# Optimization experiments

Measured on AMD Instinct MI355X. Metric: run time of the kernel, lower is better.

Reference implementation:

```python
import jax, jax.numpy as jnp
import numpy as np

B, S, D_MODEL = 2, 2048, 1024
HID, D_FF, H, WIN = 256, 512, 4, 9
LN_EPS = 1e-5


def setup_inputs() -> dict:
    key = jax.random.key(0)
    ks = jax.random.split(key, 12)
    w = lambda k, shape: jax.random.normal(k, shape, jnp.float32) * 0.02
    return dict(
        q=jax.random.normal(ks[0], (B, S, D_MODEL), jnp.float32),
        k=jax.random.normal(ks[1], (B, S, D_MODEL), jnp.float32),
        v=jax.random.normal(ks[2], (B, S, D_MODEL), jnp.float32),
        Wq=w(ks[3], (D_MODEL, HID)), bq=jnp.zeros((HID,), jnp.float32),
        Wk=w(ks[4], (D_MODEL, HID)), bk=jnp.zeros((HID,), jnp.float32),
        Wv=w(ks[5], (D_MODEL, HID)), bv=jnp.zeros((HID,), jnp.float32),
        Wo=w(ks[6], (HID, D_MODEL)), bo=jnp.zeros((D_MODEL,), jnp.float32),
        alpha=jnp.zeros((1,), jnp.float32),
        adj_w=jnp.full((1,), 0.6, jnp.float32),
        adj_b=jnp.full((1,), 0.2, jnp.float32),
        W1=w(ks[7], (D_MODEL, D_FF)), b1=jnp.zeros((D_FF,), jnp.float32),
        W2=w(ks[8], (D_FF, D_MODEL)), b2=jnp.zeros((D_MODEL,), jnp.float32),
        g1=jnp.ones((D_MODEL,), jnp.float32), be1=jnp.zeros((D_MODEL,), jnp.float32),
        g2=jnp.ones((D_MODEL,), jnp.float32), be2=jnp.zeros((D_MODEL,), jnp.float32),
    )


def _layernorm(x, g, b):
    mu = jnp.mean(x, axis=-1, keepdims=True)
    var = jnp.mean((x - mu) ** 2, axis=-1, keepdims=True)
    return (x - mu) * jax.lax.rsqrt(var + LN_EPS) * g + b


def _signed_sqrt(x):
    # sqrt(relu(x)) - sqrt(relu(-x)) with torch-style zero grad on masked branch
    p = jnp.where(x > 0, jnp.sqrt(jnp.where(x > 0, x, 1.0)), 0.0)
    n = jnp.where(x < 0, jnp.sqrt(jnp.where(x < 0, -x, 1.0)), 0.0)
    return p - n


def _local_mask(seq_len, win):
    j = jnp.arange(seq_len)[:, None]              # [S,1]
    kk = jnp.arange(win)[None, :]                 # [1,W]
    idx = jnp.clip(j - win // 2 + kk, 0, seq_len - 1)
    m = jnp.zeros((seq_len, seq_len), jnp.float32)
    return m.at[jnp.broadcast_to(j, (seq_len, win)), idx].set(1.0)


def _forward(q, k, v, Wq, bq, Wk, bk, Wv, bv, Wo, bo, alpha, adj_w, adj_b,
             W1, b1, W2, b2, g1, be1, g2, be2):
    bs, seq, _ = q.shape
    dh = HID // H
    scale = 1.0 / np.sqrt(HID)

    Q = (q @ Wq + bq).reshape(bs, seq, H, dh).transpose(0, 2, 1, 3)  # [B,H,S,dh]
    K = (k @ Wk + bk).reshape(bs, seq, H, dh).transpose(0, 2, 1, 3)
    V = (v @ Wv + bv).reshape(bs, seq, H, dh).transpose(0, 2, 1, 3)

    # distance adjacency bias: exp(-|w*d^2 - b|), d = |i-j|
    i = jnp.arange(seq, dtype=jnp.float32)
    dist = jnp.abs(i[:, None] - i[None, :])
    adj = jnp.exp(-jnp.abs(adj_w[0] * dist ** 2 - adj_b[0]))  # [S,S]

    scores = jnp.einsum('bhqd,bhkd->bhqk', Q, K) * scale + adj  # [B,H,S,S]

    mask = _local_mask(seq, WIN)                                 # [S,S]
    l_scores = jnp.where(mask == 0, -1e9, scores)

    g_map = jax.nn.softmax(scores, axis=-1)
    l_map = jax.nn.softmax(l_scores, axis=-1)

    glb = jnp.einsum('bhqk,bhkd->bqhd', g_map, V).reshape(bs, seq, HID)
    lcl = jnp.einsum('bhqk,bhkd->bqhd', l_map, V).reshape(bs, seq, HID)

    a = jax.nn.sigmoid(alpha[0])
    tmp = a * glb + (1.0 - a) * lcl

    # norm_flag: signed sqrt then F.normalize (L2 along dim=1, eps=1e-12)
    tmp = _signed_sqrt(tmp)
    nrm = jnp.maximum(jnp.sqrt(jnp.sum(tmp ** 2, axis=1, keepdims=True)), 1e-12)
    tmp = tmp / nrm

    attn_out = tmp @ Wo + bo

    x = q + attn_out
    x = _layernorm(x, g1, be1)
    # FFN (dropout inactive in eval)
    x = x + (jax.nn.relu(x @ W1 + b1) @ W2 + b2)
    x = _layernorm(x, g2, be2)
    return x


def reference(q, k, v, Wq, bq, Wk, bk, Wv, bv, Wo, bo, alpha, adj_w, adj_b,
              W1, b1, W2, b2, g1, be1, g2, be2):
    return _forward(q, k, v, Wq, bq, Wk, bk, Wv, bv, Wo, bo, alpha, adj_w,
                    adj_b, W1, b1, W2, b2, g1, be1, g2, be2)
```

## Files before the change

### kernel.cpp

```cpp
#include <hip/hip_runtime.h>

#define B_SZ   2
#define S_LEN  2048
#define DMODEL 1024
#define HID    256
#define NH     4
#define DH     64
#define DFF    512
#define LN_EPS 1e-5f
#define ATT_SCALE 0.0625f

typedef __attribute__((ext_vector_type(8))) short bf16x8;
typedef __attribute__((ext_vector_type(4))) float f32x4;

static __device__ __forceinline__ unsigned short f2bf(float x) {
    union { float f; unsigned u; } v; v.f = x;
    unsigned r = v.u + 0x7FFFu + ((v.u >> 16) & 1u);
    return (unsigned short)(r >> 16);
}
static __device__ __forceinline__ unsigned packbf(float a, float b) {
    return (unsigned)f2bf(a) | ((unsigned)f2bf(b) << 16);
}
static __device__ __forceinline__ float bf2f(unsigned short h) {
    union { unsigned u; float f; } v; v.u = ((unsigned)h) << 16; return v.f;
}
static __device__ __forceinline__ int swz(int byte) {
    return byte ^ ((byte >> 3) & 0x70);
}

#if defined(__has_builtin)
#if __has_builtin(__builtin_amdgcn_global_load_lds)
#define HAVE_GLD 1
#endif
#endif

static __device__ __forceinline__ void gld16(const void* g, void* l) {
#ifdef HAVE_GLD
    __builtin_amdgcn_global_load_lds(
        (const __attribute__((address_space(1))) void*)g,
        (__attribute__((address_space(3))) void*)l, 16, 0, 0);
#else
    *(uint4*)((char*)l + (threadIdx.x & 63) * 16) = *(const uint4*)g;
#endif
}

__device__ __forceinline__ void gstage(const unsigned short* __restrict__ G,
                                       int row0, int k0, int K, char* lds, int lane)
{
    #pragma unroll
    for (int j = 0; j < 8; ++j) {
        int o = (j * 64 + lane) * 16;
        int L = o ^ ((o >> 3) & 0x70);
        const char* ga = (const char*)G +
            ((size_t)(row0 + (L >> 7)) * K + k0) * 2 + (L & 127);
        gld16(ga, lds + j * 1024);
    }
}

__device__ __forceinline__ void gcompute(const char* As, const char* Bs,
                                         f32x4 acc[4][4], int lr, int lg)
{
    #pragma unroll
    for (int ks = 0; ks < 2; ++ks) {
        bf16x8 af[4], bfv[4];
        #pragma unroll
        for (int m = 0; m < 4; ++m) {
            int r = m * 16 + lr;
            af[m] = *(const bf16x8*)(As + ((r * 128 + ks * 64 + lg * 16) ^ ((lr & 7) << 4)));
        }
        #pragma unroll
        for (int n = 0; n < 4; ++n) {
            int r = n * 16 + lr;
            bfv[n] = *(const bf16x8*)(Bs + ((r * 128 + ks * 64 + lg * 16) ^ ((lr & 7) << 4)));
        }
        #pragma unroll
        for (int m = 0; m < 4; ++m)
            #pragma unroll
            for (int n = 0; n < 4; ++n)
                acc[m][n] = __builtin_amdgcn_mfma_f32_16x16x32_bf16(
                    af[m], bfv[n], acc[m][n], 0, 0, 0);
    }
}

__device__ __forceinline__ void gemm64_core(
    const unsigned short* __restrict__ A, const unsigned short* __restrict__ W,
    const float* __restrict__ bias, const float* __restrict__ residf,
    const unsigned short* __restrict__ residb,
    float* __restrict__ Cf, unsigned short* __restrict__ Cb,
    int N, int K, int relu, int row0, int col0)
{
    __shared__ char As0[8192], As1[8192], Bs0[8192], Bs1[8192];
    const int lane = threadIdx.x;
    const int lr = lane & 15, lg = lane >> 4;

    f32x4 acc[4][4] = {};

    gstage(A, row0, 0, K, As0, lane);
    gstage(W, col0, 0, K, Bs0, lane);
    const int NK = K >> 6;
    for (int ks = 0; ks + 2 < NK; ks += 2) {
        gstage(A, row0, (ks + 1) * 64, K, As1, lane);
        gstage(W, col0, (ks + 1) * 64, K, Bs1, lane);
        gcompute(As0, Bs0, acc, lr, lg);
        gstage(A, row0, (ks + 2) * 64, K, As0, lane);
        gstage(W, col0, (ks + 2) * 64, K, Bs0, lane);
        gcompute(As1, Bs1, acc, lr, lg);
    }
    gstage(A, row0, (NK - 1) * 64, K, As1, lane);
    gstage(W, col0, (NK - 1) * 64, K, Bs1, lane);
    gcompute(As0, Bs0, acc, lr, lg);
    gcompute(As1, Bs1, acc, lr, lg);

    #pragma unroll
    for (int mf = 0; mf < 4; ++mf) {
        #pragma unroll
        for (int nf = 0; nf < 4; ++nf) {
            #pragma unroll
            for (int r = 0; r < 4; ++r) {
                int row = row0 + mf * 16 + lg * 4 + r;
                int col = col0 + nf * 16 + lr;
                float v2 = acc[mf][nf][r] + bias[col];
                if (residf) v2 += residf[(size_t)row * N + col];
                if (residb) v2 += bf2f(residb[(size_t)row * N + col]);
                if (relu)   v2 = fmaxf(v2, 0.f);
                if (Cb) Cb[(size_t)row * N + col] = f2bf(v2);
                else    Cf[(size_t)row * N + col] = v2;
            }
        }
    }
}

__global__ __launch_bounds__(64) void gemm_b16(
    const unsigned short* __restrict__ A, const unsigned short* __restrict__ W,
    const float* __restrict__ bias, const float* __restrict__ residf,
    const unsigned short* __restrict__ residb,
    float* __restrict__ Cf, unsigned short* __restrict__ Cb,
    int N, int K, int relu)
{
    gemm64_core(A, W, bias, residf, residb, Cf, Cb, N, K, relu,
                blockIdx.x * 64, blockIdx.y * 64);
}

__global__ __launch_bounds__(64) void gemm_qkv3(
    const unsigned short* __restrict__ qkvb, const unsigned short* __restrict__ Wt,
    const float* __restrict__ bq, const float* __restrict__ bk,
    const float* __restrict__ bv, unsigned short* __restrict__ outb)
{
    const int z = blockIdx.z;
    const unsigned short* A = qkvb + (size_t)z * 4096 * 1024;
    const unsigned short* W = Wt + (size_t)z * 262144;
    const float* bias = (z == 0) ? bq : ((z == 1) ? bk : bv);
    unsigned short* Cb = outb + (size_t)z * 4096 * 256;
    gemm64_core(A, W, bias, nullptr, nullptr, nullptr, Cb, 256, 1024, 0,
                blockIdx.x * 64, blockIdx.y * 64);
}

__global__ __launch_bounds__(256) void prep_w(
    const float* __restrict__ Wq, const float* __restrict__ Wk,
    const float* __restrict__ Wv, const float* __restrict__ Wo,
    const float* __restrict__ W1, const float* __restrict__ W2,
    unsigned short* __restrict__ Wt)
{
    __shared__ float tile[64][65];
    const int bid = blockIdx.x;
    const float* src; int K, N; size_t off; int local;
    if (bid < 64)       { src = Wq; K = 1024; N = 256;  off = 0;        local = bid; }
    else if (bid < 128) { src = Wk; K = 1024; N = 256;  off = 262144;  local = bid - 64; }
    else if (bid < 192) { src = Wv; K = 1024; N = 256;  off = 524288;  local = bid - 128; }
    else if (bid < 256) { src = Wo; K = 256;  N = 1024; off = 786432;  local = bid - 192; }
    else if (bid < 384) { src = W1; K = 1024; N = 512;  off = 1048576; local = bid - 256; }
    else                { src = W2; K = 512;  N = 1024; off = 1572864; local = bid - 384; }
    const int nkt = K >> 6;
    const int k0 = (local % nkt) * 64, n0 = (local / nkt) * 64;
    const int t = threadIdx.x;
    #pragma unroll
    for (int i = 0; i < 16; ++i) {
        int id = t + i * 256;
        int r = id >> 6, c = id & 63;
        tile[r][c] = src[(size_t)(k0 + r) * N + n0 + c];
    }
    __syncthreads();
    unsigned* Wt32 = (unsigned*)(Wt + off);
    #pragma unroll
    for (int i = 0; i < 8; ++i) {
        int id = t + i * 256;
        int n = id >> 5, ku = id & 31;
        Wt32[((size_t)(n0 + n) * K + k0) / 2 + ku] =
            packbf(tile[2 * ku][n], tile[2 * ku + 1][n]);
    }
}

__global__ __launch_bounds__(256) void prep_qkv(
    const float* __restrict__ q, const float* __restrict__ k,
    const float* __restrict__ v, unsigned short* __restrict__ qkvb)
{
    const float* src = blockIdx.z == 0 ? q : (blockIdx.z == 1 ? k : v);
    uint2* dst = (uint2*)(qkvb + (size_t)blockIdx.z * 4096 * 1024);
    int idx = blockIdx.x * 256 + threadIdx.x;
    float4 x = ((const float4*)src)[idx];
    dst[idx] = make_uint2(packbf(x.x, x.y), packbf(x.z, x.w));
}

__global__ __launch_bounds__(256) void prep_v(const unsigned short* __restrict__ Vb,
                                              unsigned short* __restrict__ Vt)
{
    __shared__ unsigned Vl[64][34];
    const int k0 = blockIdx.x * 64;
    const int bh = blockIdx.y;
    const int b = bh >> 2, h = bh & 3;
    const int t = threadIdx.x;
    const unsigned* Vg = (const unsigned*)Vb + (size_t)(b * S_LEN) * 128 + h * 32;
    #pragma unroll
    for (int i = 0; i < 8; ++i) {
        int id = t + i * 256;
        int key = id >> 5, cu = id & 31;
        Vl[key][cu] = Vg[(size_t)(k0 + key) * 128 + cu];
    }
    __syncthreads();
    const unsigned short* Vl16 = (const unsigned short*)Vl;
    unsigned* Vo = (unsigned*)Vt + (size_t)bh * 65536;
    #pragma unroll
    for (int i = 0; i < 8; ++i) {
        int id = t + i * 256;
        int d = id >> 5, ku = id & 31;
        unsigned lo = Vl16[(2 * ku) * 68 + d];
        unsigned hi = Vl16[(2 * ku + 1) * 68 + d];
        Vo[(size_t)d * 1024 + (k0 >> 1) + ku] = lo | (hi << 16);
    }
}

__global__ __launch_bounds__(256) void attn_global_mfma(
    const unsigned short* __restrict__ Qb, const unsigned short* __restrict__ Kb,
    const unsigned short* __restrict__ Vt, const float* __restrict__ adj_w,
    const float* __restrict__ adj_b, unsigned short* __restrict__ glb_b)
{
    __shared__ unsigned Kl[2048];
    __shared__ unsigned Vl[2048];
    __shared__ unsigned Pl[4][512];

    const int q0 = blockIdx.x * 64;
    const int bh = blockIdx.y;
    const int b = bh >> 2, h = bh & 3;
    const int t = threadIdx.x;
    const int w = t >> 6, l = t & 63;
    const int lr = l & 15, lg = l >> 4;
    const float aw = adj_w[0], ab = adj_b[0];

    const int qrow = q0 + w * 16 + lr;
    const unsigned* qb32 = (const unsigned*)Qb + (size_t)(b * S_LEN + qrow) * 128 + h * 32;
    bf16x8 qf[2];
    #pragma unroll
    for (int hh = 0; hh < 2; ++hh) {
        union { unsigned u[4]; bf16x8 v; } tmpu;
        #pragma unroll
        for (int jj = 0; jj < 4; ++jj) tmpu.u[jj] = qb32[hh * 16 + lg * 4 + jj];
        qf[hh] = tmpu.v;
    }

    const unsigned* Kg = (const unsigned*)Kb + (size_t)(b * S_LEN) * 128 + h * 32;
    const unsigned* Vg = (const unsigned*)Vt + (size_t)bh * 65536;

    float mrow = -1e30f, lrow = 0.f;
    f32x4 o[4] = {};

    for (int k0 = 0; k0 < S_LEN; k0 += 64) {
        __syncthreads();
        #pragma unroll
        for (int i = 0; i < 2; ++i) {
            int id4 = t + i * 256;
            int r4 = id4 >> 3, c4 = id4 & 7;
            uint4 kv = *(const uint4*)(Kg + (size_t)(k0 + r4) * 128 + c4 * 4);
            *(uint4*)((char*)Kl + swz(r4 * 128 + c4 * 16)) = kv;
            uint4 vv = *(const uint4*)(Vg + (size_t)r4 * 1024 + (k0 >> 1) + c4 * 4);
            *(uint4*)((char*)Vl + swz(r4 * 128 + c4 * 16)) = vv;
        }
        __syncthreads();

        float sv[4][4];
        #pragma unroll
        for (int f = 0; f < 4; ++f) {
            int krow = f * 16 + lr;
            bf16x8 kf0 = *(const bf16x8*)((const char*)Kl + swz(krow * 128 + lg * 16));
            bf16x8 kf1 = *(const bf16x8*)((const char*)Kl + swz(krow * 128 + lg * 16 + 64));
            f32x4 stf = {0.f, 0.f, 0.f, 0.f};
            stf = __builtin_amdgcn_mfma_f32_16x16x32_bf16(kf0, qf[0], stf, 0, 0, 0);
            stf = __builtin_amdgcn_mfma_f32_16x16x32_bf16(kf1, qf[1], stf, 0, 0, 0);
            int klo = k0 + f * 16;
            bool near = (q0 + w * 16 + 15 >= klo - 6) && (q0 + w * 16 <= klo + 21);
            #pragma unroll
            for (int r = 0; r < 4; ++r) {
                float x = stf[r] * ATT_SCALE;
                if (near) {
                    int key = klo + lg * 4 + r;
                    float dd = (float)(qrow - key);
                    x += __expf(-fabsf(aw * dd * dd - ab));
                }
                sv[f][r] = x;
            }
        }

        float tmax = -1e30f;
        #pragma unroll
        for (int f = 0; f < 4; ++f)
            #pragma unroll
            for (int r = 0; r < 4; ++r) tmax = fmaxf(tmax, sv[f][r]);
        tmax = fmaxf(tmax, __shfl_xor(tmax, 16, 64));
        tmax = fmaxf(tmax, __shfl_xor(tmax, 32, 64));
        float mnew = fmaxf(mrow, tmax);
        float fac  = __expf(mrow - mnew);
        float ts = 0.f;
        #pragma unroll
        for (int f = 0; f < 4; ++f)
            #pragma unroll
            for (int r = 0; r < 4; ++r) {
                float p = __expf(sv[f][r] - mnew);
                sv[f][r] = p; ts += p;
            }
        ts += __shfl_xor(ts, 16, 64);
        ts += __shfl_xor(ts, 32, 64);
        lrow = lrow * fac + ts;
        mrow = mnew;
        #pragma unroll
        for (int rf = 0; rf < 4; ++rf) o[rf] *= fac;

        #pragma unroll
        for (int f = 0; f < 4; ++f) {
            uint2 pw;
            pw.x = packbf(sv[f][0], sv[f][1]);
            pw.y = packbf(sv[f][2], sv[f][3]);
            *(uint2*)((char*)Pl[w] + swz(lr * 128 + f * 32 + lg * 8)) = pw;
        }

        #pragma unroll
        for (int hh = 0; hh < 2; ++hh) {
            bf16x8 pf = *(const bf16x8*)((const char*)Pl[w] + swz(lr * 128 + lg * 16 + 64 * hh));
            #pragma unroll
            for (int rf = 0; rf < 4; ++rf) {
                int vrow = rf * 16 + lr;
                bf16x8 vf = *(const bf16x8*)((const char*)Vl + swz(vrow * 128 + lg * 16 + 64 * hh));
                o[rf] = __builtin_amdgcn_mfma_f32_16x16x32_bf16(vf, pf, o[rf], 0, 0, 0);
            }
        }
    }

    const float inv = 1.f / lrow;
    unsigned* gp = (unsigned*)glb_b + (((size_t)(b * S_LEN + qrow)) * NH + h) * 32;
    #pragma unroll
    for (int rf = 0; rf < 4; ++rf) {
        gp[(rf * 16 + lg * 4) >> 1]       = packbf(o[rf][0] * inv, o[rf][1] * inv);
        gp[((rf * 16 + lg * 4) >> 1) + 1] = packbf(o[rf][2] * inv, o[rf][3] * inv);
    }
}

__global__ __launch_bounds__(256) void attn_local(
    const unsigned short* __restrict__ Qb, const unsigned short* __restrict__ Kb,
    const unsigned short* __restrict__ Vb, const float* __restrict__ adj_w,
    const float* __restrict__ adj_b, unsigned short* __restrict__ lcl_b)
{
    const int wave = threadIdx.x >> 6;
    const int lane = threadIdx.x & 63;
    const int gr = blockIdx.x * 4 + wave;
    const int b = gr >> 13;
    const int rem = gr & 8191;
    const int h = rem >> 11;
    const int i = rem & 2047;
    const float w = adj_w[0], bb = adj_b[0];

    const float qd = bf2f(Qb[(size_t)(b * S_LEN + i) * HID + h * 64 + lane]);

    float sc[9]; int cls[9];
    float mx = -1e30f; int prev = -1;
    #pragma unroll
    for (int kk = 0; kk < 9; ++kk) {
        int c = i - 4 + kk;
        c = c < 0 ? 0 : (c > S_LEN - 1 ? S_LEN - 1 : c);
        bool valid = (c != prev);
        prev = c;
        float kd = bf2f(Kb[(size_t)(b * S_LEN + c) * HID + h * 64 + lane]);
        float part = qd * kd;
        #pragma unroll
        for (int off = 32; off; off >>= 1) part += __shfl_xor(part, off, 64);
        float dd = fabsf((float)(i - c));
        float vv = part * ATT_SCALE + expf(-fabsf(w * dd * dd - bb));
        sc[kk]  = valid ? vv : -1e30f;
        cls[kk] = c;
        mx = fmaxf(mx, sc[kk]);
    }
    float sum = 0.f;
    #pragma unroll
    for (int kk = 0; kk < 9; ++kk) { sc[kk] = expf(sc[kk] - mx); sum += sc[kk]; }
    const float inv = 1.f / sum;
    float o = 0.f;
    #pragma unroll
    for (int kk = 0; kk < 9; ++kk)
        o += sc[kk] * bf2f(Vb[(size_t)(b * S_LEN + cls[kk]) * HID + h * 64 + lane]);

    lcl_b[((size_t)(b * S_LEN + i)) * HID + h * 64 + lane] = f2bf(o * inv);
}

__global__ __launch_bounds__(256) void combine_ss(
    const unsigned short* __restrict__ g, const unsigned short* __restrict__ l,
    const float* __restrict__ alpha, unsigned short* __restrict__ out)
{
    const float a = 1.f / (1.f + expf(-alpha[0]));
    int idx = blockIdx.x * 256 + threadIdx.x;
    float x = a * bf2f(g[idx]) + (1.f - a) * bf2f(l[idx]);
    float r = x > 0.f ? sqrtf(x) : (x < 0.f ? -sqrtf(-x) : 0.f);
    out[idx] = f2bf(r);
}

__global__ __launch_bounds__(256) void colnorm_part(
    const unsigned short* __restrict__ tmpb, float* __restrict__ part)
{
    const int b = blockIdx.x >> 4, ch = blockIdx.x & 15;
    const int s0 = ch * 128;
    const unsigned short* base = tmpb + ((size_t)b * S_LEN + s0) * HID + threadIdx.x;
    float ss = 0.f;
    #pragma unroll 4
    for (int s = 0; s < 128; ++s) {
        float v2 = bf2f(base[(size_t)s * HID]);
        ss += v2 * v2;
    }
    part[blockIdx.x * 256 + threadIdx.x] = ss;
}

__global__ void colnorm_fin(const float* __restrict__ part, float* __restrict__ inv_nrm)
{
    const int tid = threadIdx.x;
    const int b = tid >> 8, c = tid & 255;
    float s = 0.f;
    #pragma unroll
    for (int ch = 0; ch < 16; ++ch) s += part[(b * 16 + ch) * 256 + c];
    inv_nrm[tid] = 1.f / fmaxf(sqrtf(s), 1e-12f);
}

__global__ __launch_bounds__(256) void scale_inv(
    unsigned short* __restrict__ tmpb, const float* __restrict__ inv_nrm)
{
    int idx = blockIdx.x * 256 + threadIdx.x;
    int c = idx & 255, b = idx >> 19;
    tmpb[idx] = f2bf(bf2f(tmpb[idx]) * inv_nrm[b * 256 + c]);
}

__global__ __launch_bounds__(256) void layernorm_k(
    const float* __restrict__ x, const float* __restrict__ g,
    const float* __restrict__ be, float* __restrict__ outf,
    unsigned short* __restrict__ outb)
{
    const int row = blockIdx.x;
    const float4 xv = ((const float4*)(x + (size_t)row * DMODEL))[threadIdx.x];
    float s  = xv.x + xv.y + xv.z + xv.w;
    float ss = xv.x * xv.x + xv.y * xv.y + xv.z * xv.z + xv.w * xv.w;
    #pragma unroll
    for (int off = 32; off; off >>= 1) {
        s  += __shfl_xor(s,  off, 64);
        ss += __shfl_xor(ss, off, 64);
    }
    __shared__ float rs[4], rss[4];
    if ((threadIdx.x & 63) == 0) { rs[threadIdx.x >> 6] = s; rss[threadIdx.x >> 6] = ss; }
    __syncthreads();
    s  = rs[0] + rs[1] + rs[2] + rs[3];
    ss = rss[0] + rss[1] + rss[2] + rss[3];
    const float mu  = s * (1.f / DMODEL);
    const float var = ss * (1.f / DMODEL) - mu * mu;
    const float r   = rsqrtf(var + LN_EPS);
    const float4 gv = ((const float4*)g)[threadIdx.x];
    const float4 bv = ((const float4*)be)[threadIdx.x];
    float4 ov;
    ov.x = (xv.x - mu) * r * gv.x + bv.x;
    ov.y = (xv.y - mu) * r * gv.y + bv.y;
    ov.z = (xv.z - mu) * r * gv.z + bv.z;
    ov.w = (xv.w - mu) * r * gv.w + bv.w;
    if (outf) ((float4*)(outf + (size_t)row * DMODEL))[threadIdx.x] = ov;
    if (outb) {
        unsigned* ob = (unsigned*)(outb + (size_t)row * DMODEL);
        ob[threadIdx.x * 2]     = packbf(ov.x, ov.y);
        ob[threadIdx.x * 2 + 1] = packbf(ov.z, ov.w);
    }
}

extern "C" void kernel_launch(void* const* d_in, const int* in_sizes, int n_in,
                              void* d_out, int out_size, void* d_ws, size_t ws_size,
                              hipStream_t stream)
{
    const float* q     = (const float*)d_in[0];
    const float* k     = (const float*)d_in[1];
    const float* v     = (const float*)d_in[2];
    const float* Wq    = (const float*)d_in[3];
    const float* bq    = (const float*)d_in[4];
    const float* Wk    = (const float*)d_in[5];
    const float* bk    = (const float*)d_in[6];
    const float* Wv    = (const float*)d_in[7];
    const float* bv    = (const float*)d_in[8];
    const float* Wo    = (const float*)d_in[9];
    const float* bo    = (const float*)d_in[10];
    const float* alpha = (const float*)d_in[11];
    const float* adj_w = (const float*)d_in[12];
    const float* adj_b = (const float*)d_in[13];
    const float* W1    = (const float*)d_in[14];
    const float* b1    = (const float*)d_in[15];
    const float* W2    = (const float*)d_in[16];
    const float* b2    = (const float*)d_in[17];
    const float* g1    = (const float*)d_in[18];
    const float* be1   = (const float*)d_in[19];
    const float* g2    = (const float*)d_in[20];
    const float* be2   = (const float*)d_in[21];

    const int ROWS = B_SZ * S_LEN;

    char* WS = (char*)d_ws;
    float*          x1     = (float*)WS;
    unsigned short* xlnb   = (unsigned short*)(WS + (16u << 20));
    unsigned short* glb_b  = (unsigned short*)(WS + (24u << 20));
    unsigned short* lcl_b  = (unsigned short*)(WS + (26u << 20));
    unsigned short* Qb     = (unsigned short*)(WS + (28u << 20));
    unsigned short* Kb     = (unsigned short*)(WS + (30u << 20));
    unsigned short* Vb     = (unsigned short*)(WS + (32u << 20));
    unsigned short* Vt     = (unsigned short*)(WS + (34u << 20));
    unsigned short* tmpb   = (unsigned short*)(WS + (36u << 20));
    float*          invn   = (float*)(WS + (38u << 20));
    float*          part   = (float*)(WS + (38u << 20) + 8192);
    unsigned short* Wt     = (unsigned short*)(WS + (39u << 20));
    unsigned short* hbufb  = (unsigned short*)(WS + (28u << 20));
    unsigned short* qkvb   = (unsigned short*)WS;

    prep_w<<<dim3(512), dim3(256), 0, stream>>>(Wq, Wk, Wv, Wo, W1, W2, Wt);
    prep_qkv<<<dim3(4096, 1, 3), dim3(256), 0, stream>>>(q, k, v, qkvb);
    gemm_qkv3<<<dim3(64, 4, 3), dim3(64), 0, stream>>>(qkvb, Wt, bq, bk, bv, Qb);
    prep_v<<<dim3(32, 8), dim3(256), 0, stream>>>(Vb, Vt);
    attn_global_mfma<<<dim3(32, 8), dim3(256), 0, stream>>>(Qb, Kb, Vt, adj_w, adj_b, glb_b);
    attn_local<<<dim3(4096), dim3(256), 0, stream>>>(Qb, Kb, Vb, adj_w, adj_b, lcl_b);
    combine_ss<<<dim3(4096), dim3(256), 0, stream>>>(glb_b, lcl_b, alpha, tmpb);
    colnorm_part<<<dim3(32), dim3(256), 0, stream>>>(tmpb, part);
    colnorm_fin<<<dim3(1), dim3(512), 0, stream>>>(part, invn);
    scale_inv<<<dim3(4096), dim3(256), 0, stream>>>(tmpb, invn);
    gemm_b16<<<dim3(64, 16), dim3(64), 0, stream>>>(tmpb, Wt + 786432, bo, q, nullptr,
                                                    x1, nullptr, DMODEL, HID, 0);
    layernorm_k<<<dim3(ROWS), dim3(256), 0, stream>>>(x1, g1, be1, nullptr, xlnb);
    gemm_b16<<<dim3(64, 8), dim3(64), 0, stream>>>(xlnb, Wt + 1048576, b1, nullptr, nullptr,
                                                   nullptr, hbufb, DFF, DMODEL, 1);
    gemm_b16<<<dim3(64, 16), dim3(64), 0, stream>>>(hbufb, Wt + 1572864, b2, nullptr, xlnb,
                                                    x1, nullptr, DMODEL, DFF, 0);
    layernorm_k<<<dim3(ROWS), dim3(256), 0, stream>>>(x1, g2, be2, (float*)d_out, nullptr);
}
```

Measured before the change: 323.0 us.

## Split global attention over key chunks and merge partials in combine kernel

Global attention now splits the key dimension into four chunks via a third grid dimension. Each block writes unnormalized partial outputs plus running max and sum, and a new combine kernel merges them with the local branch and signed sqrt. The aim is to fill the GPU, since the old launch used only 256 blocks. Alongside this, the GEMM staging drops async global-to-LDS loads for register prefetch into a single LDS buffer, attention K/V tiles are register-prefetched, and the column-norm partial reduction gets more blocks. The cost is extra fp32 partial traffic through memory and a lost double buffer in the GEMM.

Result: slower. 382.7 us (+18.5%).

```diff
diff --git a/kernel.cpp b/kernel.cpp
--- a/kernel.cpp
+++ b/kernel.cpp
@@ -28,32 +28,22 @@
     return byte ^ ((byte >> 3) & 0x70);
 }
 
-#if defined(__has_builtin)
-#if __has_builtin(__builtin_amdgcn_global_load_lds)
-#define HAVE_GLD 1
-#endif
-#endif
-
-static __device__ __forceinline__ void gld16(const void* g, void* l) {
-#ifdef HAVE_GLD
-    __builtin_amdgcn_global_load_lds(
-        (const __attribute__((address_space(1))) void*)g,
-        (__attribute__((address_space(3))) void*)l, 16, 0, 0);
-#else
-    *(uint4*)((char*)l + (threadIdx.x & 63) * 16) = *(const uint4*)g;
-#endif
-}
-
-__device__ __forceinline__ void gstage(const unsigned short* __restrict__ G,
-                                       int row0, int k0, int K, char* lds, int lane)
+__device__ __forceinline__ void gload16(const unsigned short* __restrict__ G,
+                                        int row0, int k0, int K, int lane, uint4 r[8])
 {
     #pragma unroll
     for (int j = 0; j < 8; ++j) {
         int o = (j * 64 + lane) * 16;
-        int L = o ^ ((o >> 3) & 0x70);
-        const char* ga = (const char*)G +
-            ((size_t)(row0 + (L >> 7)) * K + k0) * 2 + (L & 127);
-        gld16(ga, lds + j * 1024);
+        r[j] = *(const uint4*)((const char*)G +
+                ((size_t)(row0 + (o >> 7)) * K + k0) * 2 + (o & 127));
+    }
+}
+__device__ __forceinline__ void gwrite16(char* lds, int lane, const uint4 r[8])
+{
+    #pragma unroll
+    for (int j = 0; j < 8; ++j) {
+        int o = (j * 64 + lane) * 16;
+        *(uint4*)(lds + (o ^ ((o >> 3) & 0x70))) = r[j];
     }
 }
 
@@ -89,27 +79,30 @@
     float* __restrict__ Cf, unsigned short* __restrict__ Cb,
     int N, int K, int relu, int row0, int col0)
 {
-    __shared__ char As0[8192], As1[8192], Bs0[8192], Bs1[8192];
+    __shared__ char As[8192], Bs[8192];
     const int lane = threadIdx.x;
     const int lr = lane & 15, lg = lane >> 4;
 
     f32x4 acc[4][4] = {};
-
-    gstage(A, row0, 0, K, As0, lane);
-    gstage(W, col0, 0, K, Bs0, lane);
+    uint4 ra[8], rb[8];
+
+    gload16(A, row0, 0, K, lane, ra);
+    gload16(W, col0, 0, K, lane, rb);
+    gwrite16(As, lane, ra);
+    gwrite16(Bs, lane, rb);
+
     const int NK = K >> 6;
-    for (int ks = 0; ks + 2 < NK; ks += 2) {
-        gstage(A, row0, (ks + 1) * 64, K, As1, lane);
-        gstage(W, col0, (ks + 1) * 64, K, Bs1, lane);
-        gcompute(As0, Bs0, acc, lr, lg);
-        gstage(A, row0, (ks + 2) * 64, K, As0, lane);
-        gstage(W, col0, (ks + 2) * 64, K, Bs0, lane);
-        gcompute(As1, Bs1, acc, lr, lg);
-    }
-    gstage(A, row0, (NK - 1) * 64, K, As1, lane);
-    gstage(W, col0, (NK - 1) * 64, K, Bs1, lane);
-    gcompute(As0, Bs0, acc, lr, lg);
-    gcompute(As1, Bs1, acc, lr, lg);
+    for (int ks = 0; ks < NK; ++ks) {
+        if (ks + 1 < NK) {
+            gload16(A, row0, (ks + 1) * 64, K, lane, ra);
+            gload16(W, col0, (ks + 1) * 64, K, lane, rb);
+        }
+        gcompute(As, Bs, acc, lr, lg);
+        if (ks + 1 < NK) {
+            gwrite16(As, lane, ra);
+            gwrite16(Bs, lane, rb);
+        }
+    }
 
     #pragma unroll
     for (int mf = 0; mf < 4; ++mf) {
@@ -229,10 +222,11 @@
     }
 }
 
-__global__ __launch_bounds__(256) void attn_global_mfma(
+__global__ __launch_bounds__(256) void attn_global_split(
     const unsigned short* __restrict__ Qb, const unsigned short* __restrict__ Kb,
     const unsigned short* __restrict__ Vt, const float* __restrict__ adj_w,
-    const float* __restrict__ adj_b, unsigned short* __restrict__ glb_b)
+    const float* __restrict__ adj_b, float* __restrict__ Opart,
+    float* __restrict__ mlpart)
 {
     __shared__ unsigned Kl[2048];
     __shared__ unsigned Vl[2048];
@@ -240,6 +234,7 @@
 
     const int q0 = blockIdx.x * 64;
     const int bh = blockIdx.y;
+    const int ck = blockIdx.z;
     const int b = bh >> 2, h = bh & 3;
     const int t = threadIdx.x;
     const int w = t >> 6, l = t & 63;
@@ -259,22 +254,40 @@
 
     const unsigned* Kg = (const unsigned*)Kb + (size_t)(b * S_LEN) * 128 + h * 32;
     const unsigned* Vg = (const unsigned*)Vt + (size_t)bh * 65536;
+    const int kbase = ck * 512;
 
     float mrow = -1e30f, lrow = 0.f;
     f32x4 o[4] = {};
-
-    for (int k0 = 0; k0 < S_LEN; k0 += 64) {
+    uint4 rk[2], rv[2];
+
+    #pragma unroll
+    for (int i = 0; i < 2; ++i) {
+        int id4 = t + i * 256;
+        int r4 = id4 >> 3, c4 = id4 & 7;
+        rk[i] = *(const uint4*)(Kg + (size_t)(kbase + r4) * 128 + c4 * 4);
+        rv[i] = *(const uint4*)(Vg + (size_t)r4 * 1024 + (kbase >> 1) + c4 * 4);
+    }
+    #pragma unroll
+    for (int i = 0; i < 2; ++i) {
+        int id4 = t + i * 256;
+        int r4 = id4 >> 3, c4 = id4 & 7;
+        *(uint4*)((char*)Kl + swz(r4 * 128 + c4 * 16)) = rk[i];
+        *(uint4*)((char*)Vl + swz(r4 * 128 + c4 * 16)) = rv[i];
+    }
+
+    for (int tt = 0; tt < 8; ++tt) {
+        const int k0 = kbase + tt * 64;
         __syncthreads();
-        #pragma unroll
-        for (int i = 0; i < 2; ++i) {
-            int id4 = t + i * 256;
-            int r4 = id4 >> 3, c4 = id4 & 7;
-            uint4 kv = *(const uint4*)(Kg + (size_t)(k0 + r4) * 128 + c4 * 4);
-            *(uint4*)((char*)Kl + swz(r4 * 128 + c4 * 16)) = kv;
-            uint4 vv = *(const uint4*)(Vg + (size_t)r4 * 1024 + (k0 >> 1) + c4 * 4);
-            *(uint4*)((char*)Vl + swz(r4 * 128 + c4 * 16)) = vv;
-        }
-        __syncthreads();
+        if (tt < 7) {
+            const int kn = k0 + 64;
+            #pragma unroll
+            for (int i = 0; i < 2; ++i) {
+                int id4 = t + i * 256;
+                int r4 = id4 >> 3, c4 = id4 & 7;
+                rk[i] = *(const uint4*)(Kg + (size_t)(kn + r4) * 128 + c4 * 4);
+                rv[i] = *(const uint4*)(Vg + (size_t)r4 * 1024 + (kn >> 1) + c4 * 4);
+            }
+        }
 
         float sv[4][4];
         #pragma unroll
@@ -341,15 +354,62 @@
                 o[rf] = __builtin_amdgcn_mfma_f32_16x16x32_bf16(vf, pf, o[rf], 0, 0, 0);
             }
         }
-    }
-
-    const float inv = 1.f / lrow;
-    unsigned* gp = (unsigned*)glb_b + (((size_t)(b * S_LEN + qrow)) * NH + h) * 32;
-    #pragma unroll
-    for (int rf = 0; rf < 4; ++rf) {
-        gp[(rf * 16 + lg * 4) >> 1]       = packbf(o[rf][0] * inv, o[rf][1] * inv);
-        gp[((rf * 16 + lg * 4) >> 1) + 1] = packbf(o[rf][2] * inv, o[rf][3] * inv);
-    }
+
+        __syncthreads();
+        if (tt < 7) {
+            #pragma unroll
+            for (int i = 0; i < 2; ++i) {
+                int id4 = t + i * 256;
+                int r4 = id4 >> 3, c4 = id4 & 7;
+                *(uint4*)((char*)Kl + swz(r4 * 128 + c4 * 16)) = rk[i];
+                *(uint4*)((char*)Vl + swz(r4 * 128 + c4 * 16)) = rv[i];
+            }
+        }
+    }
+
+    const size_t idx = (size_t)(ck * 8 + bh) * 2048 + qrow;
+    float* op = Opart + idx * 64;
+    #pragma unroll
+    for (int rf = 0; rf < 4; ++rf)
+        *(float4*)(op + rf * 16 + lg * 4) = make_float4(o[rf][0], o[rf][1], o[rf][2], o[rf][3]);
+    if (lg == 0) {
+        mlpart[idx * 2]     = mrow;
+        mlpart[idx * 2 + 1] = lrow;
+    }
+}
+
+__global__ __launch_bounds__(256) void attn_combine(
+    const float* __restrict__ Opart, const float* __restrict__ mlpart,
+    const unsigned short* __restrict__ lcl_b, const float* __restrict__ alpha,
+    unsigned short* __restrict__ tmpb)
+{
+    const int row = blockIdx.x;
+    const int b = row >> 11;
+    const int w = threadIdx.x >> 6;
+    const int lane = threadIdx.x & 63;
+    const size_t base = (size_t)(b * NH + w) * 2048 + (row & 2047);
+
+    float mv[4], lv[4];
+    float M = -1e30f;
+    #pragma unroll
+    for (int ck = 0; ck < 4; ++ck) {
+        mv[ck] = mlpart[(ck * 16384 + base) * 2];
+        lv[ck] = mlpart[(ck * 16384 + base) * 2 + 1];
+        M = fmaxf(M, mv[ck]);
+    }
+    float O = 0.f, L = 0.f;
+    #pragma unroll
+    for (int ck = 0; ck < 4; ++ck) {
+        float e = __expf(mv[ck] - M);
+        O += e * Opart[(ck * 16384 + base) * 64 + lane];
+        L += e * lv[ck];
+    }
+    float g = O / L;
+    float lval = bf2f(lcl_b[(size_t)row * HID + w * 64 + lane]);
+    float a = 1.f / (1.f + expf(-alpha[0]));
+    float x = a * g + (1.f - a) * lval;
+    float r = x > 0.f ? sqrtf(x) : (x < 0.f ? -sqrtf(-x) : 0.f);
+    tmpb[(size_t)row * HID + w * 64 + lane] = f2bf(r);
 }
 
 __global__ __launch_bounds__(256) void attn_local(
@@ -398,26 +458,15 @@
     lcl_b[((size_t)(b * S_LEN + i)) * HID + h * 64 + lane] = f2bf(o * inv);
 }
 
-__global__ __launch_bounds__(256) void combine_ss(
-    const unsigned short* __restrict__ g, const unsigned short* __restrict__ l,
-    const float* __restrict__ alpha, unsigned short* __restrict__ out)
-{
-    const float a = 1.f / (1.f + expf(-alpha[0]));
-    int idx = blockIdx.x * 256 + threadIdx.x;
-    float x = a * bf2f(g[idx]) + (1.f - a) * bf2f(l[idx]);
-    float r = x > 0.f ? sqrtf(x) : (x < 0.f ? -sqrtf(-x) : 0.f);
-    out[idx] = f2bf(r);
-}
-
 __global__ __launch_bounds__(256) void colnorm_part(
     const unsigned short* __restrict__ tmpb, float* __restrict__ part)
 {
-    const int b = blockIdx.x >> 4, ch = blockIdx.x & 15;
-    const int s0 = ch * 128;
+    const int b = blockIdx.x >> 7, ch = blockIdx.x & 127;
+    const int s0 = ch * 16;
     const unsigned short* base = tmpb + ((size_t)b * S_LEN + s0) * HID + threadIdx.x;
     float ss = 0.f;
-    #pragma unroll 4
-    for (int s = 0; s < 128; ++s) {
+    #pragma unroll
+    for (int s = 0; s < 16; ++s) {
         float v2 = bf2f(base[(size_t)s * HID]);
         ss += v2 * v2;
     }
@@ -429,8 +478,7 @@
     const int tid = threadIdx.x;
     const int b = tid >> 8, c = tid & 255;
     float s = 0.f;
-    #pragma unroll
-    for (int ch = 0; ch < 16; ++ch) s += part[(b * 16 + ch) * 256 + c];
+    for (int ch = 0; ch < 128; ++ch) s += part[(b * 128 + ch) * 256 + c];
     inv_nrm[tid] = 1.f / fmaxf(sqrtf(s), 1e-12f);
 }
 
@@ -510,8 +558,10 @@
 
     char* WS = (char*)d_ws;
     float*          x1     = (float*)WS;
+    float*          Opart  = (float*)WS;
+    unsigned short* qkvb   = (unsigned short*)WS;
+    float*          mlpart = (float*)(WS + (16u << 20));
     unsigned short* xlnb   = (unsigned short*)(WS + (16u << 20));
-    unsigned short* glb_b  = (unsigned short*)(WS + (24u << 20));
     unsigned short* lcl_b  = (unsigned short*)(WS + (26u << 20));
     unsigned short* Qb     = (unsigned short*)(WS + (28u << 20));
     unsigned short* Kb     = (unsigned short*)(WS + (30u << 20));
@@ -519,19 +569,19 @@
     unsigned short* Vt     = (unsigned short*)(WS + (34u << 20));
     unsigned short* tmpb   = (unsigned short*)(WS + (36u << 20));
     float*          invn   = (float*)(WS + (38u << 20));
-    float*          part   = (float*)(WS + (38u << 20) + 8192);
+    float*          part   = (float*)(WS + (38u << 20) + 4096);
     unsigned short* Wt     = (unsigned short*)(WS + (39u << 20));
     unsigned short* hbufb  = (unsigned short*)(WS + (28u << 20));
-    unsigned short* qkvb   = (unsigned short*)WS;
 
     prep_w<<<dim3(512), dim3(256), 0, stream>>>(Wq, Wk, Wv, Wo, W1, W2, Wt);
     prep_qkv<<<dim3(4096, 1, 3), dim3(256), 0, stream>>>(q, k, v, qkvb);
     gemm_qkv3<<<dim3(64, 4, 3), dim3(64), 0, stream>>>(qkvb, Wt, bq, bk, bv, Qb);
     prep_v<<<dim3(32, 8), dim3(256), 0, stream>>>(Vb, Vt);
-    attn_global_mfma<<<dim3(32, 8), dim3(256), 0, stream>>>(Qb, Kb, Vt, adj_w, adj_b, glb_b);
+    attn_global_split<<<dim3(32, 8, 4), dim3(256), 0, stream>>>(Qb, Kb, Vt, adj_w, adj_b,
+                                                                Opart, mlpart);
     attn_local<<<dim3(4096), dim3(256), 0, stream>>>(Qb, Kb, Vb, adj_w, adj_b, lcl_b);
-    combine_ss<<<dim3(4096), dim3(256), 0, stream>>>(glb_b, lcl_b, alpha, tmpb);
-    colnorm_part<<<dim3(32), dim3(256), 0, stream>>>(tmpb, part);
+    attn_combine<<<dim3(4096), dim3(256), 0, stream>>>(Opart, mlpart, lcl_b, alpha, tmpb);
+    colnorm_part<<<dim3(256), dim3(256), 0, stream>>>(tmpb, part);
     colnorm_fin<<<dim3(1), dim3(512), 0, stream>>>(part, invn);
     scale_inv<<<dim3(4096), dim3(256), 0, stream>>>(tmpb, invn);
     gemm_b16<<<dim3(64, 16), dim3(64), 0, stream>>>(tmpb, Wt + 786432, bo, q, nullptr,
```
